# Kernel optimization log

Measured on AMD Instinct MI355X. Metric: run time of the kernel, lower is better.

The kernel has to match this reference:

```python
import jax, jax.numpy as jnp
import numpy as np
from jax import lax


def setup_inputs() -> dict:
    key = jax.random.key(0)
    ks = jax.random.split(key, 6)
    B, L, D, H, K = 32, 256, 16, 64, 5
    T = L - K + 1            # 252
    S = (T // 2) * H         # 8064
    return {
        "x": jax.random.normal(ks[0], (B, L, D), dtype=jnp.float32),
        "conv_w": jax.random.normal(ks[1], (D, H, K), dtype=jnp.float32) * 0.1,
        "conv_b": jax.random.normal(ks[2], (D, H), dtype=jnp.float32) * 0.1,
        "deconv_w": jax.random.normal(ks[3], (D, H, K), dtype=jnp.float32) * 0.1,
        "deconv_b": jax.random.normal(ks[4], (D,), dtype=jnp.float32) * 0.1,
        "W_attn": jax.random.normal(ks[5], (S, S), dtype=jnp.float32) * 0.01,
    }


def reference(x, conv_w, conv_b, deconv_w, deconv_b, W_attn):
    B, L, D = x.shape
    _, H, K = conv_w.shape
    T = L - K + 1
    P = T // 2
    S = P * H

    xt = jnp.transpose(x, (0, 2, 1))  # [B, D, L]
    # per-channel Conv1d(1->H) as one grouped conv: kernel [D*H, 1, K], groups=D
    y = lax.conv_general_dilated(
        xt, conv_w.reshape(D * H, 1, K), (1,), "VALID",
        dimension_numbers=("NCH", "OIH", "NCH"), feature_group_count=D,
    ) + conv_b.reshape(1, D * H, 1)
    y = jax.nn.relu(y)  # [B, D*H, T]

    # per-channel ConvTranspose1d(H->1) == full conv with flipped kernel, groups=D
    recon = lax.conv_general_dilated(
        y, deconv_w[..., ::-1], (1,), [(K - 1, K - 1)],
        dimension_numbers=("NCH", "OIH", "NCH"), feature_group_count=D,
    ) + deconv_b.reshape(1, D, 1)  # [B, D, L]

    # AvgPool1d(kernel=2, stride=2) then flatten(H, P) per channel
    pooled = y.reshape(B, D, H, P, 2).mean(axis=-1)  # [B, D, H, P]
    flat = pooled.reshape(B, D, S)                   # [B, D, S]

    main = flat[:, 0]        # [B, S]
    aux = flat[:, 1:]        # [B, D-1, S]

    # 'general' score: main . (aux @ W^T)  ==  (main @ W) . aux
    m = main @ W_attn                              # [B, S]
    scores = jnp.einsum("bt,bdt->bd", m, aux)      # [B, D-1]
    attn = jax.nn.softmax(scores, axis=-1)         # [B, D-1]
    weighted = jnp.einsum("bd,bds->bs", attn, aux)  # [B, S]

    out = jnp.concatenate([main[:, None, :], weighted[:, None, :]], axis=2)  # [B,1,2S]
    return out, attn[:, None, :], recon
```

## Files before the change

### kernel.cpp

```cpp
#include <hip/hip_runtime.h>
#include <math.h>

#define BB 32
#define LL 256
#define DD 16
#define HH 64
#define KK 5
#define TT 252
#define PP 126
#define SS 8064
#define NCHUNK 12
#define CHUNK 672
#define NKT 21

typedef __attribute__((ext_vector_type(8))) short bf16x8;
typedef __attribute__((ext_vector_type(4))) float f32x4;

__device__ __forceinline__ unsigned short f2bf(float f) {
  unsigned int u = __float_as_uint(f);
  u += 0x7FFFu + ((u >> 16) & 1u);
  return (unsigned short)(u >> 16);
}
__device__ __forceinline__ float bf2f(unsigned short h) {
  return __uint_as_float(((unsigned int)h) << 16);
}

__global__ __launch_bounds__(256) void k12_conv_recon(
    const float* __restrict__ x, const float* __restrict__ cw,
    const float* __restrict__ cb, const float* __restrict__ dw,
    const float* __restrict__ db, float* __restrict__ flat,
    unsigned short* __restrict__ mainH, unsigned short* __restrict__ mainL,
    float* __restrict__ recon) {
  __shared__ float ylds[HH * TT];
  __shared__ float xs[LL];
  __shared__ float cws[HH * KK];
  __shared__ float dws[HH * KK];
  __shared__ float cbs[HH];

  int bd = blockIdx.x;
  int b = bd / DD, d = bd % DD;
  int tid = threadIdx.x;

  {
    float4 xv = *(const float4*)(x + ((size_t)b * LL + tid) * DD + (d & ~3));
    int dl = d & 3;
    float v = (dl == 0) ? xv.x : (dl == 1) ? xv.y : (dl == 2) ? xv.z : xv.w;
    xs[tid] = v;
  }
  for (int i = tid; i < HH * KK; i += 256) {
    cws[i] = cw[(size_t)d * HH * KK + i];
    dws[i] = dw[(size_t)d * HH * KK + i];
  }
  if (tid < HH) cbs[tid] = cb[d * HH + tid];
  __syncthreads();

  {
    int h = tid >> 2, a = tid & 3;
    int t0 = a * 63;
    float w0 = cws[h * KK + 0], w1 = cws[h * KK + 1], w2 = cws[h * KK + 2],
          w3 = cws[h * KK + 3], w4 = cws[h * KK + 4];
    float bias = cbs[h];
    float x0 = xs[t0], x1 = xs[t0 + 1], x2 = xs[t0 + 2], x3 = xs[t0 + 3],
          x4 = xs[t0 + 4];
    float* yrow = ylds + h * TT + t0;
    #pragma unroll 7
    for (int t = 0; t < 63; ++t) {
      float yv = fmaf(w4, x4, fmaf(w3, x3, fmaf(w2, x2, fmaf(w1, x1, fmaf(w0, x0, bias)))));
      yrow[t] = fmaxf(yv, 0.f);
      x0 = x1; x1 = x2; x2 = x3; x3 = x4;
      if (t < 62) x4 = xs[t0 + t + 5];
    }
  }
  __syncthreads();

  for (int i = tid; i < HH * PP; i += 256) {
    int h = i / PP, p = i - h * PP;
    float pooled = 0.5f * (ylds[h * TT + 2 * p] + ylds[h * TT + 2 * p + 1]);
    flat[(size_t)bd * SS + i] = pooled;
    if (d == 0) {
      unsigned short hb = f2bf(pooled);
      mainH[(size_t)b * SS + i] = hb;
      mainL[(size_t)b * SS + i] = f2bf(pooled - bf2f(hb));
    }
  }

  {
    int l = tid;
    float acc = db[d];
    for (int h = 0; h < HH; ++h) {
      const float* yl = ylds + h * TT;
      #pragma unroll
      for (int j = 0; j < KK; ++j) {
        int t = l - j;
        if (t >= 0 && t < TT) acc = fmaf(yl[t], dws[h * KK + j], acc);
      }
    }
    recon[(size_t)bd * LL + l] = acc;
  }
}

__global__ __launch_bounds__(256) void k3_mfma(
    const float* __restrict__ W, const unsigned short* __restrict__ mainH,
    const unsigned short* __restrict__ mainL, float* __restrict__ partial) {
  __shared__ unsigned short AH[2][1024];
  __shared__ unsigned short AL[2][1024];
  __shared__ unsigned short BH[2][4096];

  int tid = threadIdx.x;
  int chunk = blockIdx.y;
  int s0 = chunk * CHUNK;
  int cbase = blockIdx.x * 128;

  int lane = tid & 63;
  int wv = tid >> 6;
  int mr = wv & 1;
  int ctb = (wv >> 1) * 4;

  f32x4 c0 = {0.f, 0.f, 0.f, 0.f};
  f32x4 c1 = {0.f, 0.f, 0.f, 0.f};
  f32x4 c2 = {0.f, 0.f, 0.f, 0.f};
  f32x4 c3 = {0.f, 0.f, 0.f, 0.f};

  int sc2 = (tid & 63) * 2;
  int sg = tid >> 6;
  const float* wbase = W + (size_t)(s0 + sg * 8) * SS + cbase + sc2;

  int ab = tid >> 2, aq = tid & 3;
  size_t abase = (size_t)ab * SS + (size_t)(s0 + aq * 8);

  int aoff  = (lane >> 4) * 256 + ((lane & 15) + 16 * mr) * 8;
  int boff0 = (lane >> 4) * 1024 + (ctb * 16 + (lane & 15)) * 8;

  float2 e0, e1, e2, e3, e4, e5, e6, e7;
  float2 o0, o1, o2, o3, o4, o5, o6, o7;
  bf16x8 aEH, aEL, aOH, aOL;

#define LOADW(R0,R1,R2,R3,R4,R5,R6,R7, KT) {                          \
    const float* p_ = wbase + (size_t)(KT) * 32 * SS;                 \
    R0 = *(const float2*)(p_);                                        \
    R1 = *(const float2*)(p_ + (size_t)SS);                           \
    R2 = *(const float2*)(p_ + 2 * (size_t)SS);                       \
    R3 = *(const float2*)(p_ + 3 * (size_t)SS);                       \
    R4 = *(const float2*)(p_ + 4 * (size_t)SS);                       \
    R5 = *(const float2*)(p_ + 5 * (size_t)SS);                       \
    R6 = *(const float2*)(p_ + 6 * (size_t)SS);                       \
    R7 = *(const float2*)(p_ + 7 * (size_t)SS); }

#define LOADA(RH, RL, KT) if (tid < 128) {                            \
    RH = *(const bf16x8*)(mainH + abase + (KT) * 32);                 \
    RL = *(const bf16x8*)(mainL + abase + (KT) * 32); }

#define CVT1(F, J) {                                                  \
    h0[J] = (short)f2bf(F.x);                                         \
    h1[J] = (short)f2bf(F.y); }

#define CVTW(R0,R1,R2,R3,R4,R5,R6,R7, BUF) {                          \
    bf16x8 h0, h1;                                                    \
    CVT1(R0, 0) CVT1(R1, 1) CVT1(R2, 2) CVT1(R3, 3)                   \
    CVT1(R4, 4) CVT1(R5, 5) CVT1(R6, 6) CVT1(R7, 7)                   \
    *(bf16x8*)&BH[BUF][sg * 1024 + sc2 * 8]     = h0;                 \
    *(bf16x8*)&BH[BUF][sg * 1024 + sc2 * 8 + 8] = h1; }

#define WRITEA(RH, RL, BUF) if (tid < 128) {                          \
    *(bf16x8*)&AH[BUF][aq * 256 + ab * 8] = RH;                       \
    *(bf16x8*)&AL[BUF][aq * 256 + ab * 8] = RL; }

#define DOMFMA(BUF) {                                                 \
    bf16x8 ah  = *(const bf16x8*)&AH[BUF][aoff];                      \
    bf16x8 al  = *(const bf16x8*)&AL[BUF][aoff];                      \
    bf16x8 bh0 = *(const bf16x8*)&BH[BUF][boff0];                     \
    bf16x8 bh1 = *(const bf16x8*)&BH[BUF][boff0 + 128];               \
    bf16x8 bh2 = *(const bf16x8*)&BH[BUF][boff0 + 256];               \
    bf16x8 bh3 = *(const bf16x8*)&BH[BUF][boff0 + 384];               \
    c0 = __builtin_amdgcn_mfma_f32_16x16x32_bf16(ah, bh0, c0, 0, 0, 0); \
    c0 = __builtin_amdgcn_mfma_f32_16x16x32_bf16(al, bh0, c0, 0, 0, 0); \
    c1 = __builtin_amdgcn_mfma_f32_16x16x32_bf16(ah, bh1, c1, 0, 0, 0); \
    c1 = __builtin_amdgcn_mfma_f32_16x16x32_bf16(al, bh1, c1, 0, 0, 0); \
    c2 = __builtin_amdgcn_mfma_f32_16x16x32_bf16(ah, bh2, c2, 0, 0, 0); \
    c2 = __builtin_amdgcn_mfma_f32_16x16x32_bf16(al, bh2, c2, 0, 0, 0); \
    c3 = __builtin_amdgcn_mfma_f32_16x16x32_bf16(ah, bh3, c3, 0, 0, 0); \
    c3 = __builtin_amdgcn_mfma_f32_16x16x32_bf16(al, bh3, c3, 0, 0, 0); }

  LOADW(e0,e1,e2,e3,e4,e5,e6,e7, 0) LOADA(aEH, aEL, 0)
  CVTW(e0,e1,e2,e3,e4,e5,e6,e7, 0) WRITEA(aEH, aEL, 0)
  LOADW(o0,o1,o2,o3,o4,o5,o6,o7, 1) LOADA(aOH, aOL, 1)
  __syncthreads();

  #pragma unroll 1
  for (int kt = 0; kt < NKT - 1; kt += 2) {
    LOADW(e0,e1,e2,e3,e4,e5,e6,e7, kt + 2) LOADA(aEH, aEL, kt + 2)
    DOMFMA(0)
    CVTW(o0,o1,o2,o3,o4,o5,o6,o7, 1) WRITEA(aOH, aOL, 1)
    __syncthreads();
    if (kt + 3 < NKT) {
      LOADW(o0,o1,o2,o3,o4,o5,o6,o7, kt + 3) LOADA(aOH, aOL, kt + 3)
    }
    DOMFMA(1)
    CVTW(e0,e1,e2,e3,e4,e5,e6,e7, 0) WRITEA(aEH, aEL, 0)
    __syncthreads();
  }
  DOMFMA(0)

  int row0 = mr * 16 + (lane >> 4) * 4;
  int col0 = cbase + ctb * 16 + (lane & 15);
  float* pp = partial + ((size_t)chunk * BB + row0) * SS + col0;
  #pragma unroll
  for (int r = 0; r < 4; ++r) pp[(size_t)r * SS]      = c0[r];
  #pragma unroll
  for (int r = 0; r < 4; ++r) pp[(size_t)r * SS + 16] = c1[r];
  #pragma unroll
  for (int r = 0; r < 4; ++r) pp[(size_t)r * SS + 32] = c2[r];
  #pragma unroll
  for (int r = 0; r < 4; ++r) pp[(size_t)r * SS + 48] = c3[r];
#undef LOADW
#undef LOADA
#undef CVT1
#undef CVTW
#undef WRITEA
#undef DOMFMA
}

__global__ __launch_bounds__(256) void k3b_reduce(
    const float4* __restrict__ partial, float4* __restrict__ m) {
  int i = blockIdx.x * 256 + threadIdx.x;
  float4 s = make_float4(0.f, 0.f, 0.f, 0.f);
  #pragma unroll
  for (int c = 0; c < NCHUNK; ++c) {
    float4 v = partial[(size_t)c * (BB * SS / 4) + i];
    s.x += v.x; s.y += v.y; s.z += v.z; s.w += v.w;
  }
  m[i] = s;
}

__global__ __launch_bounds__(256) void k4_scores(
    const float* __restrict__ m, const float* __restrict__ flat,
    float* __restrict__ scores) {
  int bd = blockIdx.x;
  int b = bd / 15, dd = bd % 15;
  const float* mb = m + (size_t)b * SS;
  const float* ab = flat + ((size_t)b * DD + 1 + dd) * SS;
  float p = 0.f;
  for (int s = threadIdx.x; s < SS; s += 256) p = fmaf(mb[s], ab[s], p);
  #pragma unroll
  for (int o = 32; o; o >>= 1) p += __shfl_xor(p, o);
  __shared__ float red[4];
  if ((threadIdx.x & 63) == 0) red[threadIdx.x >> 6] = p;
  __syncthreads();
  if (threadIdx.x == 0) scores[bd] = red[0] + red[1] + red[2] + red[3];
}

__global__ __launch_bounds__(256) void k6_out(
    const float* __restrict__ flat, const float* __restrict__ scores,
    float* __restrict__ out, float* __restrict__ attn_out) {
  int b = blockIdx.y;
  int s = blockIdx.x * 256 + threadIdx.x;

  float e0_, mx = -INFINITY;
  float sc[1]; (void)sc;
  float v0 = scores[b * 15 + 0], v1 = scores[b * 15 + 1], v2 = scores[b * 15 + 2],
        v3 = scores[b * 15 + 3], v4 = scores[b * 15 + 4], v5 = scores[b * 15 + 5],
        v6 = scores[b * 15 + 6], v7 = scores[b * 15 + 7], v8 = scores[b * 15 + 8],
        v9 = scores[b * 15 + 9], v10 = scores[b * 15 + 10], v11 = scores[b * 15 + 11],
        v12 = scores[b * 15 + 12], v13 = scores[b * 15 + 13], v14 = scores[b * 15 + 14];
  mx = fmaxf(mx, v0);  mx = fmaxf(mx, v1);  mx = fmaxf(mx, v2);
  mx = fmaxf(mx, v3);  mx = fmaxf(mx, v4);  mx = fmaxf(mx, v5);
  mx = fmaxf(mx, v6);  mx = fmaxf(mx, v7);  mx = fmaxf(mx, v8);
  mx = fmaxf(mx, v9);  mx = fmaxf(mx, v10); mx = fmaxf(mx, v11);
  mx = fmaxf(mx, v12); mx = fmaxf(mx, v13); mx = fmaxf(mx, v14);
  float a0 = expf(v0 - mx), a1 = expf(v1 - mx), a2 = expf(v2 - mx),
        a3 = expf(v3 - mx), a4 = expf(v4 - mx), a5 = expf(v5 - mx),
        a6 = expf(v6 - mx), a7 = expf(v7 - mx), a8 = expf(v8 - mx),
        a9 = expf(v9 - mx), a10 = expf(v10 - mx), a11 = expf(v11 - mx),
        a12 = expf(v12 - mx), a13 = expf(v13 - mx), a14 = expf(v14 - mx);
  float sum = a0 + a1 + a2 + a3 + a4 + a5 + a6 + a7 + a8 + a9 + a10 + a11 +
              a12 + a13 + a14;
  float inv = 1.f / sum;
  e0_ = inv; (void)e0_;

  if (blockIdx.x == 0 && threadIdx.x < 15)
    attn_out[b * 15 + threadIdx.x] =
        expf(scores[b * 15 + threadIdx.x] - mx) * inv;

  if (s >= SS) return;
  const float* fb = flat + (size_t)b * DD * SS;
  out[(size_t)b * 2 * SS + s] = fb[s];
  float w = 0.f;
  w = fmaf(a0 * inv,  fb[(size_t)1 * SS + s], w);
  w = fmaf(a1 * inv,  fb[(size_t)2 * SS + s], w);
  w = fmaf(a2 * inv,  fb[(size_t)3 * SS + s], w);
  w = fmaf(a3 * inv,  fb[(size_t)4 * SS + s], w);
  w = fmaf(a4 * inv,  fb[(size_t)5 * SS + s], w);
  w = fmaf(a5 * inv,  fb[(size_t)6 * SS + s], w);
  w = fmaf(a6 * inv,  fb[(size_t)7 * SS + s], w);
  w = fmaf(a7 * inv,  fb[(size_t)8 * SS + s], w);
  w = fmaf(a8 * inv,  fb[(size_t)9 * SS + s], w);
  w = fmaf(a9 * inv,  fb[(size_t)10 * SS + s], w);
  w = fmaf(a10 * inv, fb[(size_t)11 * SS + s], w);
  w = fmaf(a11 * inv, fb[(size_t)12 * SS + s], w);
  w = fmaf(a12 * inv, fb[(size_t)13 * SS + s], w);
  w = fmaf(a13 * inv, fb[(size_t)14 * SS + s], w);
  w = fmaf(a14 * inv, fb[(size_t)15 * SS + s], w);
  out[(size_t)b * 2 * SS + SS + s] = w;
}

extern "C" void kernel_launch(void* const* d_in, const int* in_sizes, int n_in,
                              void* d_out, int out_size, void* d_ws, size_t ws_size,
                              hipStream_t stream) {
  const float* x        = (const float*)d_in[0];
  const float* conv_w   = (const float*)d_in[1];
  const float* conv_b   = (const float*)d_in[2];
  const float* deconv_w = (const float*)d_in[3];
  const float* deconv_b = (const float*)d_in[4];
  const float* W_attn   = (const float*)d_in[5];
  float* out = (float*)d_out;

  const size_t ATTN_OFF  = (size_t)BB * 2 * SS;
  const size_t RECON_OFF = ATTN_OFF + (size_t)BB * 15;

  float* ws      = (float*)d_ws;
  float* partial = ws;
  float* flat    = partial + (size_t)NCHUNK * BB * SS;
  unsigned short* mainH = (unsigned short*)(flat + (size_t)BB * DD * SS);
  unsigned short* mainL = mainH + (size_t)BB * SS;
  float* m       = (float*)(mainL + (size_t)BB * SS);
  float* scores  = m + (size_t)BB * SS;

  k12_conv_recon<<<dim3(BB * DD), dim3(256), 0, stream>>>(
      x, conv_w, conv_b, deconv_w, deconv_b, flat, mainH, mainL, out + RECON_OFF);

  k3_mfma<<<dim3(SS / 128, NCHUNK), dim3(256), 0, stream>>>(
      W_attn, mainH, mainL, partial);

  k3b_reduce<<<dim3((BB * SS / 4) / 256), dim3(256), 0, stream>>>(
      (const float4*)partial, (float4*)m);

  k4_scores<<<dim3(BB * 15), dim3(256), 0, stream>>>(m, flat, scores);

  k6_out<<<dim3((SS + 255) / 256, BB), dim3(256), 0, stream>>>(
      flat, scores, out, out + ATTN_OFF);
}
```

Baseline: 96.88 us.

## Fuse split-K partial reduction into score kernel with per-slice partial scores

```diff
diff --git a/kernel.cpp b/kernel.cpp
--- a/kernel.cpp
+++ b/kernel.cpp
@@ -12,6 +12,8 @@
 #define NCHUNK 12
 #define CHUNK 672
 #define NKT 21
+#define NSB 8
+#define SLICE 1008
 
 typedef __attribute__((ext_vector_type(8))) short bf16x8;
 typedef __attribute__((ext_vector_type(4))) float f32x4;
@@ -220,48 +222,66 @@
 #undef DOMFMA
 }
 
-__global__ __launch_bounds__(256) void k3b_reduce(
-    const float4* __restrict__ partial, float4* __restrict__ m) {
-  int i = blockIdx.x * 256 + threadIdx.x;
-  float4 s = make_float4(0.f, 0.f, 0.f, 0.f);
-  #pragma unroll
-  for (int c = 0; c < NCHUNK; ++c) {
-    float4 v = partial[(size_t)c * (BB * SS / 4) + i];
-    s.x += v.x; s.y += v.y; s.z += v.z; s.w += v.w;
-  }
-  m[i] = s;
-}
-
 __global__ __launch_bounds__(256) void k4_scores(
-    const float* __restrict__ m, const float* __restrict__ flat,
-    float* __restrict__ scores) {
-  int bd = blockIdx.x;
-  int b = bd / 15, dd = bd % 15;
-  const float* mb = m + (size_t)b * SS;
-  const float* ab = flat + ((size_t)b * DD + 1 + dd) * SS;
-  float p = 0.f;
-  for (int s = threadIdx.x; s < SS; s += 256) p = fmaf(mb[s], ab[s], p);
-  #pragma unroll
-  for (int o = 32; o; o >>= 1) p += __shfl_xor(p, o);
-  __shared__ float red[4];
-  if ((threadIdx.x & 63) == 0) red[threadIdx.x >> 6] = p;
+    const float* __restrict__ partial, const float* __restrict__ flat,
+    float* __restrict__ pscores) {
+  int sb = blockIdx.x;
+  int b = blockIdx.y;
+  int tid = threadIdx.x;
+
+  float acc[15];
+  #pragma unroll
+  for (int dd = 0; dd < 15; ++dd) acc[dd] = 0.f;
+
+  const float* pb = partial + (size_t)b * SS;
+  const float* fb = flat + (size_t)b * DD * SS;
+
+  for (int s = sb * SLICE + tid; s < (sb + 1) * SLICE; s += 256) {
+    float mv = 0.f;
+    #pragma unroll
+    for (int c = 0; c < NCHUNK; ++c)
+      mv += pb[(size_t)c * (BB * SS) + s];
+    #pragma unroll
+    for (int dd = 0; dd < 15; ++dd)
+      acc[dd] = fmaf(mv, fb[(size_t)(1 + dd) * SS + s], acc[dd]);
+  }
+
+  #pragma unroll
+  for (int dd = 0; dd < 15; ++dd) {
+    float v = acc[dd];
+    #pragma unroll
+    for (int o = 32; o; o >>= 1) v += __shfl_xor(v, o);
+    acc[dd] = v;
+  }
+  __shared__ float red[4][15];
+  if ((tid & 63) == 0) {
+    int w = tid >> 6;
+    #pragma unroll
+    for (int dd = 0; dd < 15; ++dd) red[w][dd] = acc[dd];
+  }
   __syncthreads();
-  if (threadIdx.x == 0) scores[bd] = red[0] + red[1] + red[2] + red[3];
+  if (tid < 15)
+    pscores[(size_t)sb * (BB * 15) + b * 15 + tid] =
+        red[0][tid] + red[1][tid] + red[2][tid] + red[3][tid];
 }
 
 __global__ __launch_bounds__(256) void k6_out(
-    const float* __restrict__ flat, const float* __restrict__ scores,
+    const float* __restrict__ flat, const float* __restrict__ pscores,
     float* __restrict__ out, float* __restrict__ attn_out) {
   int b = blockIdx.y;
   int s = blockIdx.x * 256 + threadIdx.x;
 
-  float e0_, mx = -INFINITY;
-  float sc[1]; (void)sc;
-  float v0 = scores[b * 15 + 0], v1 = scores[b * 15 + 1], v2 = scores[b * 15 + 2],
-        v3 = scores[b * 15 + 3], v4 = scores[b * 15 + 4], v5 = scores[b * 15 + 5],
-        v6 = scores[b * 15 + 6], v7 = scores[b * 15 + 7], v8 = scores[b * 15 + 8],
-        v9 = scores[b * 15 + 9], v10 = scores[b * 15 + 10], v11 = scores[b * 15 + 11],
-        v12 = scores[b * 15 + 12], v13 = scores[b * 15 + 13], v14 = scores[b * 15 + 14];
+#define SUMS(DD_) ({ float t_ = 0.f;                                   \
+    _Pragma("unroll")                                                  \
+    for (int sb_ = 0; sb_ < NSB; ++sb_)                                \
+      t_ += pscores[(size_t)sb_ * (BB * 15) + b * 15 + (DD_)];         \
+    t_; })
+  float v0 = SUMS(0),  v1 = SUMS(1),  v2 = SUMS(2),  v3 = SUMS(3),
+        v4 = SUMS(4),  v5 = SUMS(5),  v6 = SUMS(6),  v7 = SUMS(7),
+        v8 = SUMS(8),  v9 = SUMS(9),  v10 = SUMS(10), v11 = SUMS(11),
+        v12 = SUMS(12), v13 = SUMS(13), v14 = SUMS(14);
+#undef SUMS
+  float mx = -INFINITY;
   mx = fmaxf(mx, v0);  mx = fmaxf(mx, v1);  mx = fmaxf(mx, v2);
   mx = fmaxf(mx, v3);  mx = fmaxf(mx, v4);  mx = fmaxf(mx, v5);
   mx = fmaxf(mx, v6);  mx = fmaxf(mx, v7);  mx = fmaxf(mx, v8);
@@ -275,11 +295,14 @@
   float sum = a0 + a1 + a2 + a3 + a4 + a5 + a6 + a7 + a8 + a9 + a10 + a11 +
               a12 + a13 + a14;
   float inv = 1.f / sum;
-  e0_ = inv; (void)e0_;
-
-  if (blockIdx.x == 0 && threadIdx.x < 15)
-    attn_out[b * 15 + threadIdx.x] =
-        expf(scores[b * 15 + threadIdx.x] - mx) * inv;
+
+  if (blockIdx.x == 0 && threadIdx.x < 15) {
+    float v = 0.f;
+    #pragma unroll
+    for (int sb_ = 0; sb_ < NSB; ++sb_)
+      v += pscores[(size_t)sb_ * (BB * 15) + b * 15 + threadIdx.x];
+    attn_out[b * 15 + threadIdx.x] = expf(v - mx) * inv;
+  }
 
   if (s >= SS) return;
   const float* fb = flat + (size_t)b * DD * SS;
@@ -322,8 +345,7 @@
   float* flat    = partial + (size_t)NCHUNK * BB * SS;
   unsigned short* mainH = (unsigned short*)(flat + (size_t)BB * DD * SS);
   unsigned short* mainL = mainH + (size_t)BB * SS;
-  float* m       = (float*)(mainL + (size_t)BB * SS);
-  float* scores  = m + (size_t)BB * SS;
+  float* pscores = (float*)(mainL + (size_t)BB * SS);
 
   k12_conv_recon<<<dim3(BB * DD), dim3(256), 0, stream>>>(
       x, conv_w, conv_b, deconv_w, deconv_b, flat, mainH, mainL, out + RECON_OFF);
@@ -331,11 +353,8 @@
   k3_mfma<<<dim3(SS / 128, NCHUNK), dim3(256), 0, stream>>>(
       W_attn, mainH, mainL, partial);
 
-  k3b_reduce<<<dim3((BB * SS / 4) / 256), dim3(256), 0, stream>>>(
-      (const float4*)partial, (float4*)m);
-
-  k4_scores<<<dim3(BB * 15), dim3(256), 0, stream>>>(m, flat, scores);
+  k4_scores<<<dim3(NSB, BB), dim3(256), 0, stream>>>(partial, flat, pscores);
 
   k6_out<<<dim3((SS + 255) / 256, BB), dim3(256), 0, stream>>>(
-      flat, scores, out, out + ATTN_OFF);
-}
+      flat, pscores, out, out + ATTN_OFF);
+}
```

Measured after the change: 89.93 us (median of 3 runs). -7.2%, faster.
